# Kernel tuning notes

Measured on AMD Instinct MI355X. Metric: run time of the kernel, lower is better.

Reference implementation:

```python
import jax, jax.numpy as jnp
import numpy as np

N_NODES = 100000

def setup_inputs() -> dict:
    key = jax.random.key(0)
    ks = jax.random.split(key, 8)
    n_feat, nhid, nclass = 256, 128, 40
    n_edges = 1600000
    x = jax.random.normal(ks[0], (N_NODES, n_feat), dtype=jnp.float32)
    edge_index = jax.random.randint(ks[1], (2, n_edges), 0, N_NODES, dtype=jnp.int64)
    # Glorot-ish scaled weights
    W1 = jax.random.normal(ks[2], (n_feat, nhid), dtype=jnp.float32) / np.sqrt(n_feat)
    b1 = jnp.zeros((nhid,), dtype=jnp.float32)
    W2 = jax.random.normal(ks[3], (nhid, nhid), dtype=jnp.float32) / np.sqrt(nhid)
    b2 = jnp.zeros((nhid,), dtype=jnp.float32)
    Wc = jax.random.normal(ks[4], (nhid, nclass), dtype=jnp.float32) / np.sqrt(nhid)
    bc = jnp.zeros((nclass,), dtype=jnp.float32)
    return {"x": x, "edge_index": edge_index, "W1": W1, "b1": b1,
            "W2": W2, "b2": b2, "Wc": Wc, "bc": bc}


def _gcn_conv(x, src, dst, W, b, n_nodes):
    """PyG GCNConv: transform, then sym-normalized aggregation with self-loops.
    out_i = sum_{j in N(i) u {i}} (d_i^-1/2 d_j^-1/2) (x_j W) + b,
    where d = in-degree over A + I.
    """
    h = x @ W  # [N, out]
    ones = jnp.ones_like(dst, dtype=h.dtype)
    deg = jax.ops.segment_sum(ones, dst, num_segments=n_nodes) + 1.0  # + self loop
    dinv = jax.lax.rsqrt(deg)  # deg >= 1, always valid
    norm = dinv[src] * dinv[dst]  # [E]
    msg = h[src] * norm[:, None]  # [E, out]  (dominant gather traffic)
    agg = jax.ops.segment_sum(msg, dst, num_segments=n_nodes)
    agg = agg + h * (dinv * dinv)[:, None]  # self-loop contribution
    return agg + b


def reference(x, edge_index, W1, b1, W2, b2, Wc, bc):
    # eval mode: dropout is identity
    src, dst = edge_index[0], edge_index[1]
    n = x.shape[0]
    h = jax.nn.relu(_gcn_conv(x, src, dst, W1, b1, n))
    h = jax.nn.relu(_gcn_conv(h, src, dst, W2, b2, n))
    return h @ Wc + bc
```

## Files before the change

### kernel.cpp

```cpp
#include <hip/hip_runtime.h>
#include <hip/hip_bf16.h>
#include <hip/hip_fp16.h>
#include <type_traits>


typedef _Float16 half8 __attribute__((ext_vector_type(8)));
typedef _Float16 half4v __attribute__((ext_vector_type(4)));
typedef float floatx4 __attribute__((ext_vector_type(4)));

#define EPB 8192


__device__ inline int block_incl_scan_256(int t, int* tmp) {
    int tid = threadIdx.x;
    tmp[tid] = t;
    __syncthreads();
    #pragma unroll
    for (int off = 1; off < 256; off <<= 1) {
        int v = (tid >= off) ? tmp[tid - off] : 0;
        __syncthreads();
        tmp[tid] += v;
        __syncthreads();
    }
    return tmp[tid];
}

template <int ITEMS>
__global__ __launch_bounds__(256) void k_scan1(const int* __restrict__ v,
                                               int* __restrict__ bsum, int n) {
    __shared__ int tmp[256];
    int base = blockIdx.x * (256 * ITEMS) + threadIdx.x * ITEMS;
    int t = 0;
    #pragma unroll
    for (int l = 0; l < ITEMS; ++l) {
        int i = base + l;
        t += (i < n) ? v[i] : 0;
    }
    block_incl_scan_256(t, tmp);
    if (threadIdx.x == 0) bsum[blockIdx.x] = tmp[255];
}

__global__ __launch_bounds__(256) void k_scan2(int* __restrict__ bsum, int nb) {
    __shared__ int tmp[256];
    int tid = threadIdx.x;
    int v = (tid < nb) ? bsum[tid] : 0;
    block_incl_scan_256(v, tmp);
    if (tid < nb) bsum[tid] = tid ? tmp[tid - 1] : 0;
}

template <int ITEMS>
__global__ __launch_bounds__(256) void k_scan3(const int* __restrict__ vin,
                                               const int* __restrict__ bsum,
                                               int* __restrict__ rp, int n) {
    __shared__ int tmp[256];
    int base = blockIdx.x * (256 * ITEMS) + threadIdx.x * ITEMS;
    int v[ITEMS];
    int t = 0;
    #pragma unroll
    for (int l = 0; l < ITEMS; ++l) {
        int i = base + l;
        v[l] = (i < n) ? vin[i] : 0;
        t += v[l];
    }
    block_incl_scan_256(t, tmp);
    int run = bsum[blockIdx.x] + (threadIdx.x ? tmp[threadIdx.x - 1] : 0);
    #pragma unroll
    for (int l = 0; l < ITEMS; ++l) {
        int i = base + l;
        if (i < n) rp[i] = run;
        run += v[l];
    }
}


__global__ __launch_bounds__(256) void k_histA(const int* __restrict__ dst,
                                               int* __restrict__ histM,
                                               int E, int nblk) {
    __shared__ int h[512];
    int tid = threadIdx.x;
    for (int i = tid; i < 512; i += 256) h[i] = 0;
    __syncthreads();
    int base = blockIdx.x * EPB;
    #pragma unroll 4
    for (int l = 0; l < EPB / 256; ++l) {
        int i = base + l * 256 + tid;
        if (i < E) atomicAdd(&h[dst[i] >> 8], 1);
    }
    __syncthreads();
    for (int i = tid; i < 512; i += 256)
        histM[i * nblk + blockIdx.x] = h[i];
}

__global__ __launch_bounds__(256) void k_scatterA(const int* __restrict__ src,
                                                  const int* __restrict__ dst,
                                                  const int* __restrict__ histS,
                                                  unsigned long long* __restrict__ eB,
                                                  int E, int nblk) {
    __shared__ int bse[512];
    __shared__ int cnt[512];
    int tid = threadIdx.x;
    for (int i = tid; i < 512; i += 256) {
        bse[i] = histS[i * nblk + blockIdx.x];
        cnt[i] = 0;
    }
    __syncthreads();
    int base = blockIdx.x * EPB;
    #pragma unroll 4
    for (int l = 0; l < EPB / 256; ++l) {
        int i = base + l * 256 + tid;
        if (i < E) {
            int d = dst[i];
            int s = src[i];
            int b = d >> 8;
            int r = atomicAdd(&cnt[b], 1);
            eB[bse[b] + r] = ((unsigned long long)(unsigned)d << 32) | (unsigned)s;
        }
    }
}

#define BCAP 4608
__global__ __launch_bounds__(256) void k_sortB(const unsigned long long* __restrict__ eB,
                                               const int* __restrict__ histS,
                                               int* __restrict__ srcS,
                                               int* __restrict__ rowptr,
                                               float* __restrict__ dinv,
                                               int n, int E, int nblk) {
    const int b   = blockIdx.x;
    const int tid = threadIdx.x;
    const int ni0 = b << 8;
    int s0 = histS[b * nblk];
    int s1 = (b < 511) ? histS[(b + 1) * nblk] : E;
    int cnt = s1 - s0;
    if (cnt > BCAP) cnt = BCAP;
    if (cnt == 0 && ni0 > n) return;

    __shared__ int hist[256];
    __shared__ int tmp[256];
    __shared__ int baseA[256];
    __shared__ int cntA[256];
    __shared__ int dstL[BCAP];
    __shared__ unsigned srcL[BCAP];
    __shared__ int lbA[256];

    hist[tid] = 0;
    cntA[tid] = 0;
    __syncthreads();
    for (int i = s0 + tid; i < s0 + cnt; i += 256) {
        int d = (int)(eB[i] >> 32);
        atomicAdd(&hist[d & 255], 1);
    }
    __syncthreads();
    int own  = hist[tid];
    int incl = block_incl_scan_256(own, tmp);
    baseA[tid] = incl - own;
    __syncthreads();
    for (int i = s0 + tid; i < s0 + cnt; i += 256) {
        unsigned long long v = eB[i];
        int d = (int)(v >> 32);
        int dig = d & 255;
        int r = atomicAdd(&cntA[dig], 1);
        int pos = baseA[dig] + r;
        dstL[pos] = d;
        srcL[pos] = (unsigned)v;
    }
    __syncthreads();
    for (int j = tid; j < cnt; j += 256)
        srcS[s0 + j] = (int)srcL[j];
    if (ni0 <= n) {
        int i = ni0 + tid;
        int lo = 0, hi = cnt;
        while (lo < hi) {
            int mid = (lo + hi) >> 1;
            if (dstL[mid] < i) lo = mid + 1; else hi = mid;
        }
        lbA[tid] = lo;
        __syncthreads();
        if (i <= n) {
            rowptr[i] = s0 + lo;
            if (i < n) {
                int ub = (tid < 255) ? lbA[tid + 1] : cnt;
                dinv[i] = rsqrtf((float)(ub - lo + 1));
            }
        }
    }
}

__global__ __launch_bounds__(256) void k_wcast(const float* __restrict__ W,
                                               _Float16* __restrict__ Wt,
                                               int N, int K, int kbits, int total) {
    int i = blockIdx.x * 256 + threadIdx.x;
    if (i < total) {
        int c = i >> kbits;
        int k = i & (K - 1);
        Wt[i] = (c < N) ? (_Float16)W[(size_t)k * N + c] : (_Float16)0.f;
    }
}


template <int K, int BN, typename AT, typename OT>
__global__ __launch_bounds__(256) void gemm_mfma(const AT* __restrict__ A,
                                                 const _Float16* __restrict__ Wt,
                                                 const float* __restrict__ bias,
                                                 OT* __restrict__ C,
                                                 int M, int N) {
    constexpr int NT = BN / 16;
    __shared__ __align__(16) _Float16 As[64][40];
    __shared__ __align__(16) _Float16 Bs[BN][40];

    const int tid  = threadIdx.x;
    const int bm   = blockIdx.x * 64;
    const int lane = tid & 63;
    const int wv   = tid >> 6;
    const int qd   = lane >> 4;
    const int ln15 = lane & 15;

    floatx4 acc[NT];
    #pragma unroll
    for (int c = 0; c < NT; ++c) acc[c] = (floatx4){0.f, 0.f, 0.f, 0.f};

    for (int k0 = 0; k0 < K; k0 += 32) {
        if constexpr (std::is_same<AT, float>::value) {
            #pragma unroll
            for (int l = 0; l < 2; ++l) {
                int f4  = tid + l * 256;
                int row = f4 >> 3;
                int kk  = (f4 & 7) << 2;
                float4 v = make_float4(0.f, 0.f, 0.f, 0.f);
                if (bm + row < M)
                    v = *(const float4*)(A + (size_t)(bm + row) * K + k0 + kk);
                half4v h;
                h[0] = (_Float16)v.x; h[1] = (_Float16)v.y;
                h[2] = (_Float16)v.z; h[3] = (_Float16)v.w;
                *(half4v*)&As[row][kk] = h;
            }
        } else {
            int row = tid >> 2;
            int kk  = (tid & 3) << 3;
            uint4 v = make_uint4(0u, 0u, 0u, 0u);
            if (bm + row < M)
                v = *(const uint4*)((const _Float16*)A + (size_t)(bm + row) * K + k0 + kk);
            *(uint4*)&As[row][kk] = v;
        }
        #pragma unroll
        for (int l = 0; l < (BN * 4 + 255) / 256; ++l) {
            int idx = tid + l * 256;
            if (idx < BN * 4) {
                int col = idx >> 2;
                int kk  = (idx & 3) << 3;
                *(uint4*)&Bs[col][kk] =
                    *(const uint4*)(Wt + (size_t)col * K + k0 + kk);
            }
        }
        __syncthreads();

        half8 a = *(const half8*)&As[wv * 16 + ln15][qd * 8];
        #pragma unroll
        for (int c = 0; c < NT; ++c) {
            half8 b = *(const half8*)&Bs[c * 16 + ln15][qd * 8];
            acc[c] = __builtin_amdgcn_mfma_f32_16x16x32_f16(a, b, acc[c], 0, 0, 0);
        }
        __syncthreads();
    }

    int baseRow = bm + wv * 16 + qd * 4;
    #pragma unroll
    for (int c = 0; c < NT; ++c) {
        int col = c * 16 + ln15;
        if constexpr (std::is_same<OT, _Float16>::value) {
            #pragma unroll
            for (int r = 0; r < 4; ++r) {
                int row = baseRow + r;
                if (row < M) C[(size_t)row * N + col] = (_Float16)acc[c][r];
            }
        } else {
            float bv = (col < N && bias) ? bias[col] : 0.f;
            #pragma unroll
            for (int r = 0; r < 4; ++r) {
                int row = baseRow + r;
                if (row < M && col < N)
                    ((float*)C)[(size_t)row * N + col] = acc[c][r] + bv;
            }
        }
    }
}


static __device__ __forceinline__ float2 h2f2(unsigned int raw) {
    __half2 h = *(__half2*)&raw;
    return __half22float2(h);
}

__global__ __launch_bounds__(256) void gcn_agg(const unsigned int* __restrict__ h,
                                               const int* __restrict__ rowptr,
                                               const int* __restrict__ srcS,
                                               const float* __restrict__ dinv,
                                               const float* __restrict__ bias,
                                               unsigned int* __restrict__ out,
                                               int n, int do_relu) {
    int node = blockIdx.x * 4 + (threadIdx.x >> 6);
    if (node >= n) return;
    int lane = threadIdx.x & 63;

    float di = dinv[node];
    float2 v = h2f2(h[(size_t)node * 64 + lane]);
    float s  = di * di;
    float accx = v.x * s;
    float accy = v.y * s;

    int e0 = rowptr[node];
    int e1 = rowptr[node + 1];

    for (int ce = e0; ce < e1; ce += 64) {
        int cnt = e1 - ce;
        cnt = (cnt < 64) ? cnt : 64;
        int colv = 0, wval = 0;
        if (lane < cnt) {
            int c = srcS[ce + lane];
            colv = c;
            wval = __float_as_int(di * dinv[c]);
        }
        int d = 0;
        for (; d + 4 <= cnt; d += 4) {
            int c0 = __builtin_amdgcn_readlane(colv, d + 0);
            int c1 = __builtin_amdgcn_readlane(colv, d + 1);
            int c2 = __builtin_amdgcn_readlane(colv, d + 2);
            int c3 = __builtin_amdgcn_readlane(colv, d + 3);
            float w0 = __int_as_float(__builtin_amdgcn_readlane(wval, d + 0));
            float w1 = __int_as_float(__builtin_amdgcn_readlane(wval, d + 1));
            float w2 = __int_as_float(__builtin_amdgcn_readlane(wval, d + 2));
            float w3 = __int_as_float(__builtin_amdgcn_readlane(wval, d + 3));
            unsigned r0 = h[(size_t)(unsigned)c0 * 64 + lane];
            unsigned r1 = h[(size_t)(unsigned)c1 * 64 + lane];
            unsigned r2 = h[(size_t)(unsigned)c2 * 64 + lane];
            unsigned r3 = h[(size_t)(unsigned)c3 * 64 + lane];
            float2 u0 = h2f2(r0);
            float2 u1 = h2f2(r1);
            float2 u2 = h2f2(r2);
            float2 u3 = h2f2(r3);
            accx += u0.x * w0;
            accy += u0.y * w0;
            accx += u1.x * w1;
            accy += u1.y * w1;
            accx += u2.x * w2;
            accy += u2.y * w2;
            accx += u3.x * w3;
            accy += u3.y * w3;
        }
        for (; d < cnt; ++d) {
            int c = __builtin_amdgcn_readlane(colv, d);
            float w = __int_as_float(__builtin_amdgcn_readlane(wval, d));
            float2 u = h2f2(h[(size_t)(unsigned)c * 64 + lane]);
            accx += u.x * w;
            accy += u.y * w;
        }
    }

    float2 b = ((const float2*)bias)[lane];
    float ox = accx + b.x;
    float oy = accy + b.y;
    if (do_relu) {
        ox = fmaxf(ox, 0.f);
        oy = fmaxf(oy, 0.f);
    }
    __half2 p = __floats2half2_rn(ox, oy);
    out[(size_t)node * 64 + lane] = *(unsigned int*)&p;
}


extern "C" void kernel_launch(void* const* d_in, const int* in_sizes, int n_in,
                              void* d_out, int out_size, void* d_ws, size_t ws_size,
                              hipStream_t stream) {
    const float* x  = (const float*)d_in[0];
    const int* eidx = (const int*)d_in[1];
    const float* W1 = (const float*)d_in[2];
    const float* b1 = (const float*)d_in[3];
    const float* W2 = (const float*)d_in[4];
    const float* b2 = (const float*)d_in[5];
    const float* Wc = (const float*)d_in[6];
    const float* bc = (const float*)d_in[7];
    float* out = (float*)d_out;

    const int NF = 256, NH = 128, NC = 40;
    const int n = in_sizes[0] / NF;
    const int E = in_sizes[1] / 2;
    const int* src = eidx;
    const int* dst = eidx + E;

    const int nblk = (E + EPB - 1) / EPB;
    const int hm   = 512 * nblk;
    const int nbA  = (hm + 4095) / 4096;

    char* wsb = (char*)d_ws;
    size_t off = 0;
    auto alloc = [&](size_t bytes) {
        char* p = wsb + off;
        off = (off + bytes + 511) & ~(size_t)511;
        return p;
    };
    _Float16* hbuf = (_Float16*)alloc((size_t)n * NH * 2);
    _Float16* abuf = (_Float16*)alloc((size_t)n * NH * 2);
    _Float16* W1t  = (_Float16*)alloc((size_t)128 * 256 * 2);
    _Float16* W2t  = (_Float16*)alloc((size_t)128 * 128 * 2);
    _Float16* Wct  = (_Float16*)alloc((size_t)48 * 128 * 2);
    unsigned long long* eB = (unsigned long long*)alloc((size_t)E * 8);
    int* srcS      = (int*)alloc((size_t)E * 4);
    int* histM     = (int*)alloc((size_t)hm * 4);
    int* histS     = (int*)alloc((size_t)hm * 4);
    int* rowptr    = (int*)alloc((size_t)(n + 1) * 4);
    float* dinv    = (float*)alloc((size_t)n * 4);
    int* bsumA     = (int*)alloc(1024);

    k_histA<<<nblk, 256, 0, stream>>>(dst, histM, E, nblk);
    k_scan1<16><<<nbA, 256, 0, stream>>>(histM, bsumA, hm);
    k_scan2<<<1, 256, 0, stream>>>(bsumA, nbA);
    k_scan3<16><<<nbA, 256, 0, stream>>>(histM, bsumA, histS, hm);
    k_scatterA<<<nblk, 256, 0, stream>>>(src, dst, histS, eB, E, nblk);
    k_sortB<<<512, 256, 0, stream>>>(eB, histS, srcS, rowptr, dinv, n, E, nblk);

    k_wcast<<<(128 * 256 + 255) / 256, 256, 0, stream>>>(W1, W1t, 128, 256, 8, 128 * 256);
    k_wcast<<<(128 * 128 + 255) / 256, 256, 0, stream>>>(W2, W2t, 128, 128, 7, 128 * 128);
    k_wcast<<<(48 * 128 + 255) / 256, 256, 0, stream>>>(Wc, Wct, 40, 128, 7, 48 * 128);

    const int gMt = (n + 63) / 64;
    gemm_mfma<256, 128, float, _Float16><<<gMt, 256, 0, stream>>>(x, W1t, nullptr, hbuf, n, NH);
    gcn_agg<<<(n + 3) / 4, 256, 0, stream>>>((const unsigned int*)hbuf, rowptr, srcS, dinv, b1,
                                             (unsigned int*)abuf, n, 1);
    gemm_mfma<128, 128, _Float16, _Float16><<<gMt, 256, 0, stream>>>(abuf, W2t, nullptr, hbuf, n, NH);
    gcn_agg<<<(n + 3) / 4, 256, 0, stream>>>((const unsigned int*)hbuf, rowptr, srcS, dinv, b2,
                                             (unsigned int*)abuf, n, 1);
    gemm_mfma<128, 48, _Float16, float><<<gMt, 256, 0, stream>>>(abuf, Wct, bc, out, n, NC);
}
```

Measured before the change: 422.3 us.

## Gather four neighbor rows per wave with 16-byte half8 loads in aggregation

The GCN aggregation kernel now splits each 64-lane wave into four 16-lane groups. Each group handles a different edge, and each lane loads 8 fp16 features with a single 16-byte load, where before the whole wave loaded one row with 4-byte loads. The four partial sums are combined at the end with xor shuffles, and only group 0 writes the result. Neighbor indices and weights are distributed with ds_bpermute instead of readlane. The goal is more memory-level parallelism and fewer, wider gather instructions. The cost is extra shuffle reductions and wasted loads of row 0 on padded tail edges.

```diff
diff --git a/kernel.cpp b/kernel.cpp
--- a/kernel.cpp
+++ b/kernel.cpp
@@ -285,11 +285,6 @@
 }
 
 
-static __device__ __forceinline__ float2 h2f2(unsigned int raw) {
-    __half2 h = *(__half2*)&raw;
-    return __half22float2(h);
-}
-
 __global__ __launch_bounds__(256) void gcn_agg(const unsigned int* __restrict__ h,
                                                const int* __restrict__ rowptr,
                                                const int* __restrict__ srcS,
@@ -299,16 +294,24 @@
                                                int n, int do_relu) {
     int node = blockIdx.x * 4 + (threadIdx.x >> 6);
     if (node >= n) return;
-    int lane = threadIdx.x & 63;
+    const int lane = threadIdx.x & 63;
+    const int g    = lane >> 4;
+    const int t    = lane & 15;
+
+    const _Float16* hb = (const _Float16*)h;
 
     float di = dinv[node];
-    float2 v = h2f2(h[(size_t)node * 64 + lane]);
-    float s  = di * di;
-    float accx = v.x * s;
-    float accy = v.y * s;
-
     int e0 = rowptr[node];
     int e1 = rowptr[node + 1];
+
+    half8 sv = *(const half8*)(hb + (size_t)(unsigned)node * 128 + t * 8);
+    const float4* b4 = (const float4*)bias;
+    float4 blo = b4[t * 2 + 0];
+    float4 bhi = b4[t * 2 + 1];
+
+    float acc[8];
+    #pragma unroll
+    for (int i = 0; i < 8; ++i) acc[i] = 0.f;
 
     for (int ce = e0; ce < e1; ce += 64) {
         int cnt = e1 - ce;
@@ -319,51 +322,34 @@
             colv = c;
             wval = __float_as_int(di * dinv[c]);
         }
-        int d = 0;
-        for (; d + 4 <= cnt; d += 4) {
-            int c0 = __builtin_amdgcn_readlane(colv, d + 0);
-            int c1 = __builtin_amdgcn_readlane(colv, d + 1);
-            int c2 = __builtin_amdgcn_readlane(colv, d + 2);
-            int c3 = __builtin_amdgcn_readlane(colv, d + 3);
-            float w0 = __int_as_float(__builtin_amdgcn_readlane(wval, d + 0));
-            float w1 = __int_as_float(__builtin_amdgcn_readlane(wval, d + 1));
-            float w2 = __int_as_float(__builtin_amdgcn_readlane(wval, d + 2));
-            float w3 = __int_as_float(__builtin_amdgcn_readlane(wval, d + 3));
-            unsigned r0 = h[(size_t)(unsigned)c0 * 64 + lane];
-            unsigned r1 = h[(size_t)(unsigned)c1 * 64 + lane];
-            unsigned r2 = h[(size_t)(unsigned)c2 * 64 + lane];
-            unsigned r3 = h[(size_t)(unsigned)c3 * 64 + lane];
-            float2 u0 = h2f2(r0);
-            float2 u1 = h2f2(r1);
-            float2 u2 = h2f2(r2);
-            float2 u3 = h2f2(r3);
-            accx += u0.x * w0;
-            accy += u0.y * w0;
-            accx += u1.x * w1;
-            accy += u1.y * w1;
-            accx += u2.x * w2;
-            accy += u2.y * w2;
-            accx += u3.x * w3;
-            accy += u3.y * w3;
-        }
-        for (; d < cnt; ++d) {
-            int c = __builtin_amdgcn_readlane(colv, d);
-            float w = __int_as_float(__builtin_amdgcn_readlane(wval, d));
-            float2 u = h2f2(h[(size_t)(unsigned)c * 64 + lane]);
-            accx += u.x * w;
-            accy += u.y * w;
-        }
-    }
-
-    float2 b = ((const float2*)bias)[lane];
-    float ox = accx + b.x;
-    float oy = accy + b.y;
-    if (do_relu) {
-        ox = fmaxf(ox, 0.f);
-        oy = fmaxf(oy, 0.f);
-    }
-    __half2 p = __floats2half2_rn(ox, oy);
-    out[(size_t)node * 64 + lane] = *(unsigned int*)&p;
+        #pragma unroll 2
+        for (int d = 0; d < cnt; d += 4) {
+            int idx = (d + g) << 2;
+            int c   = __builtin_amdgcn_ds_bpermute(idx, colv);
+            float w = __int_as_float(__builtin_amdgcn_ds_bpermute(idx, wval));
+            half8 hv = *(const half8*)(hb + (size_t)(unsigned)c * 128 + t * 8);
+            #pragma unroll
+            for (int i = 0; i < 8; ++i)
+                acc[i] += (float)hv[i] * w;
+        }
+    }
+
+    #pragma unroll
+    for (int i = 0; i < 8; ++i) acc[i] += __shfl_xor(acc[i], 16);
+    #pragma unroll
+    for (int i = 0; i < 8; ++i) acc[i] += __shfl_xor(acc[i], 32);
+
+    float s = di * di;
+    float bb[8] = {blo.x, blo.y, blo.z, blo.w, bhi.x, bhi.y, bhi.z, bhi.w};
+    half8 o;
+    #pragma unroll
+    for (int i = 0; i < 8; ++i) {
+        float v = acc[i] + (float)sv[i] * s + bb[i];
+        if (do_relu) v = fmaxf(v, 0.f);
+        o[i] = (_Float16)v;
+    }
+    if (g == 0)
+        *(half8*)((_Float16*)out + (size_t)(unsigned)node * 128 + t * 8) = o;
 }
 
 
```

Result: no change. 418.1 us (-1.0%).
